# Kernel tuning notes

Hardware: AMD Instinct MI355X
Metric: run time of the kernel (lower is better)

The kernel has to match this reference:

```python
import jax, jax.numpy as jnp
import numpy as np

B, H, CI, O = 8, 16, 16, 16          # batch, child spatial, child caps, parent caps
K, S, ROUTINGS = 3, 1, 3             # kernel, stride, EM iterations
FINAL_LAMBDA = 0.01
EPS = 1e-9


def setup_inputs() -> dict:
    key = jax.random.key(0)
    k1, k2, k3, k4, k5 = jax.random.split(key, 5)
    inputs_pose = jax.random.normal(k1, (B, H, H, CI, 16), dtype=jnp.float32)
    inputs_activation = jax.random.uniform(k2, (B, H, H, CI, 1), dtype=jnp.float32)
    # transformation matrices: [1, k*k*child_caps, parent_caps, 4, 4]
    w = jax.random.normal(k3, (1, K * K * CI, O, 4, 4), dtype=jnp.float32)
    beta_a = jax.random.normal(k4, (O,), dtype=jnp.float32)
    beta_v = jax.random.normal(k5, (O,), dtype=jnp.float32)
    return {"inputs_pose": inputs_pose, "inputs_activation": inputs_activation,
            "w": w, "beta_a": beta_a, "beta_v": beta_v}


def _extract_patches(x, k, s):
    # kernel_tile: im2col-like gather. x: [B, H, W, ...] -> [B, p, p, k, k, ...]
    Hs = x.shape[1]
    p = (Hs - k) // s + 1
    idx = (jnp.arange(p) * s)[:, None] + jnp.arange(k)[None, :]      # [p, k]
    xh = x[:, idx]                   # [B, ph, kh, W, ...]
    patches = xh[:, :, :, idx]       # [B, ph, kh, pw, kw, ...]
    return jnp.swapaxes(patches, 2, 3), p


def _child_index_map(Hs, k, s, p):
    # flat child spatial index feeding each (parent pos, kernel slot)
    ph = np.arange(p)[:, None] * s + np.arange(k)[None, :]           # [p, k]
    ch = ph[:, None, :, None] * Hs + ph[None, :, None, :]            # [p, p, k, k]
    return ch.reshape(p * p, k * k)                                   # [P2, K2]


def reference(inputs_pose, inputs_activation, w, beta_a, beta_v):
    P = (H - K) // S + 1
    P2, K2 = P * P, K * K
    K2CI = K2 * CI

    # ---- kernel_tile ----
    pose_t, _ = _extract_patches(inputs_pose, K, S)       # [B,P,P,K,K,CI,16]
    act_t, _ = _extract_patches(inputs_activation, K, S)  # [B,P,P,K,K,CI,1]
    pose_unroll = pose_t.reshape(B * P2, K2CI, 4, 4)
    act_unroll = act_t.reshape(B * P2, K2CI)

    # ---- compute_votes: tiny 4x4 matmuls per (child slot, parent cap) ----
    votes = jnp.einsum('nkpq,koqr->nkopr', pose_unroll, w[0])  # [B*P2,K2CI,O,4,4]
    votes = votes.reshape(B, P2, K2CI, O, 16)
    act_i = act_unroll.reshape(B, P2, K2CI, 1, 1)

    # ---- spatial routing bookkeeping (static integers) ----
    child_idx = _child_index_map(H, K, S, P)                    # [P2, K2]
    kk_child = np.repeat(child_idx, CI, axis=1)                 # [P2, K2CI]
    counts = np.zeros(H * H, np.float32)
    np.add.at(counts, child_idx.reshape(-1), 1.0)               # parents per child pos
    cap_id = np.tile(np.arange(CI), K2)                         # [K2CI]
    seg = jnp.asarray((kk_child * CI + cap_id[None, :]).reshape(-1))  # [P2*K2CI]
    n_seg = H * H * CI

    # initial routing: uniform over all (parent pos, parent cap) each child feeds
    rr0 = 1.0 / (O * counts[kk_child])                          # [P2, K2CI]
    rr = jnp.asarray(rr0)[None, :, :, None, None]               # bcast [1,P2,K2CI,1,1]

    beta_a_b = beta_a.reshape(1, 1, 1, O, 1)
    beta_v_b = beta_v.reshape(1, 1, 1, O, 1)

    mean = act_j = None
    for it in range(ROUTINGS):
        inv_temp = FINAL_LAMBDA * (1.0 - 0.95 ** (it + 1))
        # ---- M-step: weighted Gaussian statistics ----
        rr_prime = rr * act_i                                   # [B,P2,K2CI,O,1]
        rr_sum = jnp.sum(rr_prime, axis=2, keepdims=True) + EPS # [B,P2,1,O,1]
        mean = jnp.sum(rr_prime * votes, axis=2, keepdims=True) / rr_sum
        var = jnp.sum(rr_prime * jnp.square(votes - mean), axis=2, keepdims=True) / rr_sum + EPS
        cost_h = (beta_v_b + 0.5 * jnp.log(var)) * rr_sum       # [B,P2,1,O,16]
        cost = jnp.sum(cost_h, axis=-1, keepdims=True)          # [B,P2,1,O,1]
        act_j = jax.nn.sigmoid(inv_temp * (beta_a_b - cost))    # [B,P2,1,O,1]
        # ---- E-step: softmax over all (parent pos, parent cap) per child capsule ----
        if it < ROUTINGS - 1:
            log_p = -0.5 * jnp.sum(jnp.square(votes - mean) / var
                                   + jnp.log(2.0 * np.pi * var), axis=-1)  # [B,P2,K2CI,O]
            zz = jnp.log(act_j[..., 0] + EPS) + log_p           # [B,P2,K2CI,O]
            z = jnp.transpose(zz, (1, 2, 0, 3)).reshape(P2 * K2CI, B, O)
            row_max = jnp.max(z, axis=-1)                       # [P2*K2CI, B]
            seg_max = jax.ops.segment_max(row_max, seg, num_segments=n_seg)
            g = seg_max[seg][..., None]
            ez = jnp.exp(z - g)
            denom = jax.ops.segment_sum(jnp.sum(ez, axis=-1), seg, num_segments=n_seg)[seg]
            rr_new = ez / (denom[..., None] + EPS)              # sums to 1 per child capsule
            rr = jnp.transpose(rr_new.reshape(P2, K2CI, B, O), (2, 0, 1, 3))[..., None]

    pose_out = mean[:, :, 0].reshape(B, P, P, O, 16)
    act_out = act_j[:, :, 0].reshape(B, P, P, O, 1)
    return pose_out, act_out
```

## Files before the change

kernel.cpp:

```cpp
#include <hip/hip_runtime.h>

namespace {
constexpr int B_ = 8, H_ = 16, CI_ = 16, O_ = 16, P_ = 14;
constexpr int P2_ = P_ * P_;
constexpr int K2CI_ = 144;
constexpr int NV_ = 2304;
constexpr float EPS_ = 1e-9f;
constexpr float LOG2PI_ = 1.8378770664093453f;

__device__ __forceinline__ float cnt1(int h) {
  int lo = (h - (P_ - 1)) > 0 ? (h - (P_ - 1)) : 0;
  int hi = h < 2 ? h : 2;
  return (float)(hi - lo + 1);
}

__global__ __launch_bounds__(256) void transpose_w(const float* __restrict__ w,
                                                   float* __restrict__ wt) {
  const int i = blockIdx.x * 256 + threadIdx.x;
  const int ko = i >> 4, q = (i >> 2) & 3, r = i & 3;
  wt[(ko << 4) + (r << 2) + q] = w[i];
}

template <int MODE>
__global__ __launch_bounds__(512, 8) void caps_main(
    const float* __restrict__ pose, const float* __restrict__ act,
    const float* __restrict__ wt, const float* __restrict__ beta_a,
    const float* __restrict__ beta_v, const float* __restrict__ zin,
    const float* __restrict__ gmax, const float* __restrict__ gden,
    float* __restrict__ zout, float* __restrict__ out) {
  __shared__ float rr_s[(MODE == 0) ? K2CI_ : NV_];
  __shared__ float part[9][512];
  __shared__ float gm_s[(MODE == 0) ? 1 : K2CI_];
  __shared__ float ad_s[(MODE == 0) ? 1 : K2CI_];

  const int tid = threadIdx.x;
  const int wv = __builtin_amdgcn_readfirstlane(tid >> 6);
  const int l = tid & 63;
  const int o = l >> 2, r = l & 3;
  const int pid = blockIdx.x;
  const int b = pid / P2_;
  const int p2 = pid - b * P2_;
  const int pi = p2 / P_;
  const int pj = p2 - pi * P_;
  const float inv_temp = (MODE == 0) ? 0.0005f : (MODE == 1) ? 0.000975f : 0.00142625f;

  if (MODE == 0) {
    if (tid < K2CI_) {
      const int ci = tid & 15, kk = tid >> 4;
      const int ki = (kk >= 6) ? 2 : (kk >= 3) ? 1 : 0, kj = kk - 3 * ki;
      const int cidx = ((b * H_ + pi + ki) * H_ + pj + kj) * CI_ + ci;
      rr_s[tid] = act[cidx] / (16.0f * cnt1(pi + ki) * cnt1(pj + kj));
    }
  } else {
    if (tid < K2CI_) {
      const int ci = tid & 15, kk = tid >> 4;
      const int ki = (kk >= 6) ? 2 : (kk >= 3) ? 1 : 0, kj = kk - 3 * ki;
      const int cidx = ((b * H_ + pi + ki) * H_ + pj + kj) * CI_ + ci;
      gm_s[tid] = gmax[cidx];
      ad_s[tid] = act[cidx] / (gden[cidx] + EPS_);
    }
    __syncthreads();
    for (int i4 = tid; i4 < NV_ / 4; i4 += 512) {
      const float4 z4 = ((const float4*)(zin + (size_t)pid * NV_))[i4];
      const int k = i4 >> 2;
      const float gmk = gm_s[k], adk = ad_s[k];
      float4 r4;
      r4.x = __expf(z4.x - gmk) * adk;
      r4.y = __expf(z4.y - gmk) * adk;
      r4.z = __expf(z4.z - gmk) * adk;
      r4.w = __expf(z4.w - gmk) * adk;
      ((float4*)rr_s)[i4] = r4;
    }
  }
  __syncthreads();

  const float bvo = 16.0f * beta_v[o];
  const float bao = beta_a[o];

  const float* pose_b = pose + ((size_t)((b * H_ + pi) * H_ + pj) << 8);
  const float* wt_l = wt + (l << 2);
  const int ci0 = wv * 2;

  float prr = 0.f;
  float pm0 = 0.f, pm1 = 0.f, pm2 = 0.f, pm3 = 0.f;
  float pv0 = 0.f, pv1 = 0.f, pv2 = 0.f, pv3 = 0.f;
#pragma unroll
  for (int kk = 0; kk < 9; ++kk) {
    const int ki = kk / 3, kj = kk - 3 * (kk / 3);
    const float* pb = pose_b + ((ki * H_ + kj) << 8);
    const float* wb = wt_l + ((size_t)kk << 12);
#pragma unroll
    for (int c = 0; c < 2; ++c) {
      const int ci = ci0 + c;
      const float4 w4 = *(const float4*)(wb + (ci << 8));
      const float4 Pa = *(const float4*)(pb + (ci << 4));
      const float4 Pb = *(const float4*)(pb + (ci << 4) + 4);
      const float4 Pc = *(const float4*)(pb + (ci << 4) + 8);
      const float4 Pd = *(const float4*)(pb + (ci << 4) + 12);
      const float v0 = Pa.x * w4.x + Pa.y * w4.y + Pa.z * w4.z + Pa.w * w4.w;
      const float v1 = Pb.x * w4.x + Pb.y * w4.y + Pb.z * w4.z + Pb.w * w4.w;
      const float v2 = Pc.x * w4.x + Pc.y * w4.y + Pc.z * w4.z + Pc.w * w4.w;
      const float v3 = Pd.x * w4.x + Pd.y * w4.y + Pd.z * w4.z + Pd.w * w4.w;
      const float rrk =
          (MODE == 0) ? rr_s[kk * 16 + ci] : rr_s[((kk * 16 + ci) << 4) + o];
      prr += rrk;
      const float a0 = rrk * v0, a1 = rrk * v1, a2 = rrk * v2, a3 = rrk * v3;
      pm0 += a0; pm1 += a1; pm2 += a2; pm3 += a3;
      pv0 = fmaf(a0, v0, pv0); pv1 = fmaf(a1, v1, pv1);
      pv2 = fmaf(a2, v2, pv2); pv3 = fmaf(a3, v3, pv3);
    }
  }
  part[0][tid] = prr;
  part[1][tid] = pm0; part[2][tid] = pm1; part[3][tid] = pm2; part[4][tid] = pm3;
  part[5][tid] = pv0; part[6][tid] = pv1; part[7][tid] = pv2; part[8][tid] = pv3;
  __syncthreads();
  float s[9];
#pragma unroll
  for (int j = 0; j < 9; ++j) {
    float acc = part[j][l];
#pragma unroll
    for (int wvi = 1; wvi < 8; ++wvi) acc += part[j][wvi * 64 + l];
    s[j] = acc;
  }
  const float rsum = s[0] + EPS_;
  const float irs = 1.0f / rsum;
  const float m0 = s[1] * irs, m1 = s[2] * irs, m2 = s[3] * irs, m3 = s[4] * irs;
  const float va0 = fmaxf(s[5] * irs - m0 * m0, 0.f) + EPS_;
  const float va1 = fmaxf(s[6] * irs - m1 * m1, 0.f) + EPS_;
  const float va2 = fmaxf(s[7] * irs - m2 * m2, 0.f) + EPS_;
  const float va3 = fmaxf(s[8] * irs - m3 * m3, 0.f) + EPS_;
  float slv = __logf(va0) + __logf(va1) + __logf(va2) + __logf(va3);
  slv += __shfl_xor(slv, 1);
  slv += __shfl_xor(slv, 2);
  const float cost = (bvo + 0.5f * slv) * rsum;
  const float aj = 1.0f / (1.0f + __expf(-inv_temp * (bao - cost)));

  if (MODE == 2) {
    if (wv == 0) {
      float* ob = out + ((size_t)(pid * 16 + o) << 4) + r;
      ob[0] = m0; ob[4] = m1; ob[8] = m2; ob[12] = m3;
      if (r == 0) out[(size_t)B_ * P2_ * O_ * 16 + pid * 16 + o] = aj;
    }
    return;
  }

  const float iv0 = 1.0f / va0, iv1 = 1.0f / va1, iv2 = 1.0f / va2, iv3 = 1.0f / va3;
  const float Cz = __logf(aj + EPS_) - 0.5f * (slv + 16.0f * LOG2PI_);
  float* zo = zout + (size_t)pid * NV_ + o;
#pragma unroll
  for (int kk = 0; kk < 9; ++kk) {
    const int ki = kk / 3, kj = kk - 3 * (kk / 3);
    const float* pb = pose_b + ((ki * H_ + kj) << 8);
    const float* wb = wt_l + ((size_t)kk << 12);
#pragma unroll
    for (int c = 0; c < 2; ++c) {
      const int ci = ci0 + c;
      const float4 w4 = *(const float4*)(wb + (ci << 8));
      const float4 Pa = *(const float4*)(pb + (ci << 4));
      const float4 Pb = *(const float4*)(pb + (ci << 4) + 4);
      const float4 Pc = *(const float4*)(pb + (ci << 4) + 8);
      const float4 Pd = *(const float4*)(pb + (ci << 4) + 12);
      const float v0 = Pa.x * w4.x + Pa.y * w4.y + Pa.z * w4.z + Pa.w * w4.w;
      const float v1 = Pb.x * w4.x + Pb.y * w4.y + Pb.z * w4.z + Pb.w * w4.w;
      const float v2 = Pc.x * w4.x + Pc.y * w4.y + Pc.z * w4.z + Pc.w * w4.w;
      const float v3 = Pd.x * w4.x + Pd.y * w4.y + Pd.z * w4.z + Pd.w * w4.w;
      const float d0 = v0 - m0, d1 = v1 - m1, d2 = v2 - m2, d3 = v3 - m3;
      float q = d0 * d0 * iv0 + d1 * d1 * iv1 + d2 * d2 * iv2 + d3 * d3 * iv3;
      q += __shfl_xor(q, 1);
      q += __shfl_xor(q, 2);
      if (r == 0) zo[(kk * 16 + ci) << 4] = Cz - 0.5f * q;
    }
  }
}

__global__ __launch_bounds__(256) void seg_reduce(const float* __restrict__ z,
                                                  float* __restrict__ gmax,
                                                  float* __restrict__ gden) {
  const int tid = blockIdx.x * 256 + threadIdx.x;
  const int part = tid & 3, ci = (tid >> 2) & 15, w2 = (tid >> 6) & 15;
  const int h = (tid >> 10) & 15, b = tid >> 14;
  float4 v[9];
  float m = -3.0e38f;
#pragma unroll
  for (int s = 0; s < 9; ++s) {
    const int ki = (s >= 6) ? 2 : (s >= 3) ? 1 : 0, kj = s - 3 * ki;
    const int pi = h - ki, pj = w2 - kj;
    if ((unsigned)pi < (unsigned)P_ && (unsigned)pj < (unsigned)P_) {
      v[s] = *(const float4*)(z + (size_t)(b * P2_ + pi * P_ + pj) * NV_ + s * 256 +
                              ci * 16 + part * 4);
    } else {
      v[s] = make_float4(-3.0e38f, -3.0e38f, -3.0e38f, -3.0e38f);
    }
    m = fmaxf(m, fmaxf(fmaxf(v[s].x, v[s].y), fmaxf(v[s].z, v[s].w)));
  }
  m = fmaxf(m, __shfl_xor(m, 1));
  m = fmaxf(m, __shfl_xor(m, 2));
  float s_ = 0.f;
#pragma unroll
  for (int s = 0; s < 9; ++s) {
    s_ += __expf(v[s].x - m) + __expf(v[s].y - m) + __expf(v[s].z - m) + __expf(v[s].w - m);
  }
  s_ += __shfl_xor(s_, 1);
  s_ += __shfl_xor(s_, 2);
  if (part == 0) {
    gmax[tid >> 2] = m;
    gden[tid >> 2] = s_;
  }
}
}

extern "C" void kernel_launch(void* const* d_in, const int* in_sizes, int n_in,
                              void* d_out, int out_size, void* d_ws, size_t ws_size,
                              hipStream_t stream) {
  const float* pose = (const float*)d_in[0];
  const float* act = (const float*)d_in[1];
  const float* w = (const float*)d_in[2];
  const float* ba = (const float*)d_in[3];
  const float* bv = (const float*)d_in[4];
  float* out = (float*)d_out;

  float* z = (float*)d_ws;
  float* gm = z + (size_t)B_ * P2_ * NV_;
  float* gd = gm + B_ * H_ * H_ * CI_;
  float* wt = gd + B_ * H_ * H_ * CI_;

  const int NB = B_ * P2_;
  transpose_w<<<144, 256, 0, stream>>>(w, wt);
  caps_main<0><<<NB, 512, 0, stream>>>(pose, act, wt, ba, bv, z, gm, gd, z, out);
  seg_reduce<<<512, 256, 0, stream>>>(z, gm, gd);
  caps_main<1><<<NB, 512, 0, stream>>>(pose, act, wt, ba, bv, z, gm, gd, z, out);
  seg_reduce<<<512, 256, 0, stream>>>(z, gm, gd);
  caps_main<2><<<NB, 512, 0, stream>>>(pose, act, wt, ba, bv, z, gm, gd, z, out);
}
```

Measured before the change: 174.7 us.

## Transpose pose to column-major and vectorize vote math with packed float2 FMAs

Adds a pre-pass that transposes each 4x4 pose matrix into a workspace buffer, so the vote computation can use packed 2-wide FMA on pairs of rows (v_pk_fma style) instead of scalar dot products. Accumulators and the mean/variance math are converted to float2 vectors. The cross-wave reduction is now split across 320 threads writing to a small shared buffer, rather than every thread redundantly summing all 9 partials. This adds an extra kernel launch and extra workspace traffic for the transposed pose.

```diff
diff --git a/kernel.cpp b/kernel.cpp
--- a/kernel.cpp
+++ b/kernel.cpp
@@ -8,6 +8,8 @@
 constexpr float EPS_ = 1e-9f;
 constexpr float LOG2PI_ = 1.8378770664093453f;
 
+using f2 = __attribute__((ext_vector_type(2))) float;
+
 __device__ __forceinline__ float cnt1(int h) {
   int lo = (h - (P_ - 1)) > 0 ? (h - (P_ - 1)) : 0;
   int hi = h < 2 ? h : 2;
@@ -21,15 +23,42 @@
   wt[(ko << 4) + (r << 2) + q] = w[i];
 }
 
+__global__ __launch_bounds__(256) void transpose_pose(const float* __restrict__ pose,
+                                                      float* __restrict__ pose_t) {
+  const int i = blockIdx.x * 256 + threadIdx.x;
+  const int cell = i >> 4, idx = i & 15;
+  const int p = idx >> 2, q = idx & 3;
+  pose_t[(cell << 4) + (q << 2) + p] = pose[i];
+}
+
+__device__ __forceinline__ void vote_dot(const float* __restrict__ pb, const float4 w4,
+                                         f2& v01, f2& v23) {
+  const f2 A0 = *(const f2*)(pb + 0), B0 = *(const f2*)(pb + 2);
+  const f2 A1 = *(const f2*)(pb + 4), B1 = *(const f2*)(pb + 6);
+  const f2 A2 = *(const f2*)(pb + 8), B2 = *(const f2*)(pb + 10);
+  const f2 A3 = *(const f2*)(pb + 12), B3 = *(const f2*)(pb + 14);
+  v01 = A0 * w4.x;
+  v23 = B0 * w4.x;
+  v01 = __builtin_elementwise_fma(A1, (f2){w4.y, w4.y}, v01);
+  v23 = __builtin_elementwise_fma(B1, (f2){w4.y, w4.y}, v23);
+  v01 = __builtin_elementwise_fma(A2, (f2){w4.z, w4.z}, v01);
+  v23 = __builtin_elementwise_fma(B2, (f2){w4.z, w4.z}, v23);
+  v01 = __builtin_elementwise_fma(A3, (f2){w4.w, w4.w}, v01);
+  v23 = __builtin_elementwise_fma(B3, (f2){w4.w, w4.w}, v23);
+}
+
 template <int MODE>
 __global__ __launch_bounds__(512, 8) void caps_main(
-    const float* __restrict__ pose, const float* __restrict__ act,
+    const float* __restrict__ pose_t, const float* __restrict__ act,
     const float* __restrict__ wt, const float* __restrict__ beta_a,
     const float* __restrict__ beta_v, const float* __restrict__ zin,
     const float* __restrict__ gmax, const float* __restrict__ gden,
     float* __restrict__ zout, float* __restrict__ out) {
   __shared__ float rr_s[(MODE == 0) ? K2CI_ : NV_];
-  __shared__ float part[9][512];
+  __shared__ f2 partv[4][512];
+  __shared__ float partr[512];
+  __shared__ f2 sfin[4][64];
+  __shared__ float sfr[64];
   __shared__ float gm_s[(MODE == 0) ? 1 : K2CI_];
   __shared__ float ad_s[(MODE == 0) ? 1 : K2CI_];
 
@@ -77,59 +106,64 @@
   const float bvo = 16.0f * beta_v[o];
   const float bao = beta_a[o];
 
-  const float* pose_b = pose + ((size_t)((b * H_ + pi) * H_ + pj) << 8);
+  const float* pose_b = pose_t + ((size_t)((b * H_ + pi) * H_ + pj) << 8);
   const float* wt_l = wt + (l << 2);
   const int ci0 = wv * 2;
 
   float prr = 0.f;
-  float pm0 = 0.f, pm1 = 0.f, pm2 = 0.f, pm3 = 0.f;
-  float pv0 = 0.f, pv1 = 0.f, pv2 = 0.f, pv3 = 0.f;
+  f2 pm01 = {0.f, 0.f}, pm23 = {0.f, 0.f}, pv01 = {0.f, 0.f}, pv23 = {0.f, 0.f};
 #pragma unroll
   for (int kk = 0; kk < 9; ++kk) {
     const int ki = kk / 3, kj = kk - 3 * (kk / 3);
-    const float* pb = pose_b + ((ki * H_ + kj) << 8);
+    const float* pbase = pose_b + ((ki * H_ + kj) << 8);
     const float* wb = wt_l + ((size_t)kk << 12);
 #pragma unroll
     for (int c = 0; c < 2; ++c) {
       const int ci = ci0 + c;
       const float4 w4 = *(const float4*)(wb + (ci << 8));
-      const float4 Pa = *(const float4*)(pb + (ci << 4));
-      const float4 Pb = *(const float4*)(pb + (ci << 4) + 4);
-      const float4 Pc = *(const float4*)(pb + (ci << 4) + 8);
-      const float4 Pd = *(const float4*)(pb + (ci << 4) + 12);
-      const float v0 = Pa.x * w4.x + Pa.y * w4.y + Pa.z * w4.z + Pa.w * w4.w;
-      const float v1 = Pb.x * w4.x + Pb.y * w4.y + Pb.z * w4.z + Pb.w * w4.w;
-      const float v2 = Pc.x * w4.x + Pc.y * w4.y + Pc.z * w4.z + Pc.w * w4.w;
-      const float v3 = Pd.x * w4.x + Pd.y * w4.y + Pd.z * w4.z + Pd.w * w4.w;
+      f2 v01, v23;
+      vote_dot(pbase + (ci << 4), w4, v01, v23);
       const float rrk =
           (MODE == 0) ? rr_s[kk * 16 + ci] : rr_s[((kk * 16 + ci) << 4) + o];
       prr += rrk;
-      const float a0 = rrk * v0, a1 = rrk * v1, a2 = rrk * v2, a3 = rrk * v3;
-      pm0 += a0; pm1 += a1; pm2 += a2; pm3 += a3;
-      pv0 = fmaf(a0, v0, pv0); pv1 = fmaf(a1, v1, pv1);
-      pv2 = fmaf(a2, v2, pv2); pv3 = fmaf(a3, v3, pv3);
-    }
-  }
-  part[0][tid] = prr;
-  part[1][tid] = pm0; part[2][tid] = pm1; part[3][tid] = pm2; part[4][tid] = pm3;
-  part[5][tid] = pv0; part[6][tid] = pv1; part[7][tid] = pv2; part[8][tid] = pv3;
+      const f2 rr2 = {rrk, rrk};
+      const f2 a01 = rr2 * v01, a23 = rr2 * v23;
+      pm01 += a01;
+      pm23 += a23;
+      pv01 = __builtin_elementwise_fma(a01, v01, pv01);
+      pv23 = __builtin_elementwise_fma(a23, v23, pv23);
+    }
+  }
+  partv[0][tid] = pm01; partv[1][tid] = pm23;
+  partv[2][tid] = pv01; partv[3][tid] = pv23;
+  partr[tid] = prr;
   __syncthreads();
-  float s[9];
-#pragma unroll
-  for (int j = 0; j < 9; ++j) {
-    float acc = part[j][l];
-#pragma unroll
-    for (int wvi = 1; wvi < 8; ++wvi) acc += part[j][wvi * 64 + l];
-    s[j] = acc;
-  }
-  const float rsum = s[0] + EPS_;
+  if (tid < 320) {
+    if (tid < 256) {
+      const int st = tid >> 6, li = tid & 63;
+      f2 acc = partv[st][li];
+#pragma unroll
+      for (int wvi = 1; wvi < 8; ++wvi) acc += partv[st][wvi * 64 + li];
+      sfin[st][li] = acc;
+    } else {
+      const int li = tid & 63;
+      float acc = partr[li];
+#pragma unroll
+      for (int wvi = 1; wvi < 8; ++wvi) acc += partr[wvi * 64 + li];
+      sfr[li] = acc;
+    }
+  }
+  __syncthreads();
+  const f2 S01 = sfin[0][l], S23 = sfin[1][l];
+  const f2 V01 = sfin[2][l], V23 = sfin[3][l];
+  const float rsum = sfr[l] + EPS_;
   const float irs = 1.0f / rsum;
-  const float m0 = s[1] * irs, m1 = s[2] * irs, m2 = s[3] * irs, m3 = s[4] * irs;
-  const float va0 = fmaxf(s[5] * irs - m0 * m0, 0.f) + EPS_;
-  const float va1 = fmaxf(s[6] * irs - m1 * m1, 0.f) + EPS_;
-  const float va2 = fmaxf(s[7] * irs - m2 * m2, 0.f) + EPS_;
-  const float va3 = fmaxf(s[8] * irs - m3 * m3, 0.f) + EPS_;
-  float slv = __logf(va0) + __logf(va1) + __logf(va2) + __logf(va3);
+  const f2 irs2 = {irs, irs};
+  const f2 m01 = S01 * irs2, m23 = S23 * irs2;
+  const f2 zero2 = {0.f, 0.f}, eps2 = {EPS_, EPS_};
+  const f2 va01 = __builtin_elementwise_max(V01 * irs2 - m01 * m01, zero2) + eps2;
+  const f2 va23 = __builtin_elementwise_max(V23 * irs2 - m23 * m23, zero2) + eps2;
+  float slv = __logf(va01.x) + __logf(va01.y) + __logf(va23.x) + __logf(va23.y);
   slv += __shfl_xor(slv, 1);
   slv += __shfl_xor(slv, 2);
   const float cost = (bvo + 0.5f * slv) * rsum;
@@ -138,34 +172,30 @@
   if (MODE == 2) {
     if (wv == 0) {
       float* ob = out + ((size_t)(pid * 16 + o) << 4) + r;
-      ob[0] = m0; ob[4] = m1; ob[8] = m2; ob[12] = m3;
+      ob[0] = m01.x; ob[4] = m01.y; ob[8] = m23.x; ob[12] = m23.y;
       if (r == 0) out[(size_t)B_ * P2_ * O_ * 16 + pid * 16 + o] = aj;
     }
     return;
   }
 
-  const float iv0 = 1.0f / va0, iv1 = 1.0f / va1, iv2 = 1.0f / va2, iv3 = 1.0f / va3;
+  const f2 iv01 = {1.0f / va01.x, 1.0f / va01.y};
+  const f2 iv23 = {1.0f / va23.x, 1.0f / va23.y};
   const float Cz = __logf(aj + EPS_) - 0.5f * (slv + 16.0f * LOG2PI_);
   float* zo = zout + (size_t)pid * NV_ + o;
 #pragma unroll
   for (int kk = 0; kk < 9; ++kk) {
     const int ki = kk / 3, kj = kk - 3 * (kk / 3);
-    const float* pb = pose_b + ((ki * H_ + kj) << 8);
+    const float* pbase = pose_b + ((ki * H_ + kj) << 8);
     const float* wb = wt_l + ((size_t)kk << 12);
 #pragma unroll
     for (int c = 0; c < 2; ++c) {
       const int ci = ci0 + c;
       const float4 w4 = *(const float4*)(wb + (ci << 8));
-      const float4 Pa = *(const float4*)(pb + (ci << 4));
-      const float4 Pb = *(const float4*)(pb + (ci << 4) + 4);
-      const float4 Pc = *(const float4*)(pb + (ci << 4) + 8);
-      const float4 Pd = *(const float4*)(pb + (ci << 4) + 12);
-      const float v0 = Pa.x * w4.x + Pa.y * w4.y + Pa.z * w4.z + Pa.w * w4.w;
-      const float v1 = Pb.x * w4.x + Pb.y * w4.y + Pb.z * w4.z + Pb.w * w4.w;
-      const float v2 = Pc.x * w4.x + Pc.y * w4.y + Pc.z * w4.z + Pc.w * w4.w;
-      const float v3 = Pd.x * w4.x + Pd.y * w4.y + Pd.z * w4.z + Pd.w * w4.w;
-      const float d0 = v0 - m0, d1 = v1 - m1, d2 = v2 - m2, d3 = v3 - m3;
-      float q = d0 * d0 * iv0 + d1 * d1 * iv1 + d2 * d2 * iv2 + d3 * d3 * iv3;
+      f2 v01, v23;
+      vote_dot(pbase + (ci << 4), w4, v01, v23);
+      const f2 d01 = v01 - m01, d23 = v23 - m23;
+      const f2 q2 = __builtin_elementwise_fma(d01 * d01, iv01, (d23 * d23) * iv23);
+      float q = q2.x + q2.y;
       q += __shfl_xor(q, 1);
       q += __shfl_xor(q, 2);
       if (r == 0) zo[(kk * 16 + ci) << 4] = Cz - 0.5f * q;
@@ -223,12 +253,14 @@
   float* gm = z + (size_t)B_ * P2_ * NV_;
   float* gd = gm + B_ * H_ * H_ * CI_;
   float* wt = gd + B_ * H_ * H_ * CI_;
+  float* pt = wt + 36864;
 
   const int NB = B_ * P2_;
   transpose_w<<<144, 256, 0, stream>>>(w, wt);
-  caps_main<0><<<NB, 512, 0, stream>>>(pose, act, wt, ba, bv, z, gm, gd, z, out);
+  transpose_pose<<<2048, 256, 0, stream>>>(pose, pt);
+  caps_main<0><<<NB, 512, 0, stream>>>(pt, act, wt, ba, bv, z, gm, gd, z, out);
   seg_reduce<<<512, 256, 0, stream>>>(z, gm, gd);
-  caps_main<1><<<NB, 512, 0, stream>>>(pose, act, wt, ba, bv, z, gm, gd, z, out);
+  caps_main<1><<<NB, 512, 0, stream>>>(pt, act, wt, ba, bv, z, gm, gd, z, out);
   seg_reduce<<<512, 256, 0, stream>>>(z, gm, gd);
-  caps_main<2><<<NB, 512, 0, stream>>>(pose, act, wt, ba, bv, z, gm, gd, z, out);
-}
+  caps_main<2><<<NB, 512, 0, stream>>>(pt, act, wt, ba, bv, z, gm, gd, z, out);
+}
```

After: 166.1 us. 1.05x faster.
